# Kernel optimization log

Measured on AMD Instinct MI355X. Metric: run time of the kernel, lower is better.

The kernel has to match this reference:

```python
import math
import jax, jax.numpy as jnp
import numpy as np

DIM = 1024
QK_DIM = 200
HIDDEN = 2 * DIM  # expansion_factor = 2
N = 8192


def setup_inputs() -> dict:
    key = jax.random.key(0)
    ks = jax.random.split(key, 8)
    s = 0.02
    return {
        "x": jax.random.normal(ks[0], (N, DIM), dtype=jnp.float32),
        "W_hidden": jax.random.normal(ks[1], (DIM, 2 * HIDDEN), dtype=jnp.float32) * s,
        "b_hidden": jnp.zeros((2 * HIDDEN,), dtype=jnp.float32),
        "W_qk": jax.random.normal(ks[2], (DIM, QK_DIM), dtype=jnp.float32) * s,
        "b_qk": jnp.zeros((QK_DIM,), dtype=jnp.float32),
        "gamma": 1.0 + jax.random.normal(ks[3], (2, QK_DIM), dtype=jnp.float32) * s,
        "beta": jnp.zeros((2, QK_DIM), dtype=jnp.float32),
        "W_out": jax.random.normal(ks[4], (HIDDEN, DIM), dtype=jnp.float32) * s,
        "b_out": jnp.zeros((DIM,), dtype=jnp.float32),
    }


def reference(x, W_hidden, b_hidden, W_qk, b_qk, gamma, beta, W_out, b_out):
    # to_hidden: Linear(dim -> 2*hidden) + SiLU, then chunk into v, gate
    hid = jax.nn.silu(x @ W_hidden + b_hidden)        # [N, 2H]
    v, gate = jnp.split(hid, 2, axis=-1)              # [N, H] each
    # to_qk: Linear(dim -> qk_dim) + SiLU
    qk = jax.nn.silu(x @ W_qk + b_qk)                 # [N, qk]
    # OffsetScale (heads=2): per-head affine on the shared qk
    q = qk * gamma[0] + beta[0]                       # [N, qk]
    k = qk * gamma[1] + beta[1]                       # [N, qk]
    # scores scaled by sqrt(dim) (module uses self.dim, not qk_dim)
    sim = (q @ k.T) * (1.0 / math.sqrt(x.shape[-1]))  # [N, N]
    # ReLU-squared attention (no softmax); dropout=0.0 -> identity
    attn = jnp.square(jax.nn.relu(sim))
    out = attn @ v                                    # [N, H]
    out = out * gate
    out = out @ W_out + b_out                         # [N, dim]
    # add_residual=True in this module multiplies by x
    return out * x
```

## Files before the change

### kernel.cpp

```cpp
#include <hip/hip_runtime.h>
#include <stdint.h>


typedef __bf16 bf16x8 __attribute__((ext_vector_type(8)));
typedef float f32x4 __attribute__((ext_vector_type(4)));

__device__ __forceinline__ uint16_t f2bf(float f) {
  uint32_t u = __builtin_bit_cast(uint32_t, f);
  u += 0x7fffu + ((u >> 16) & 1u);
  return (uint16_t)(u >> 16);
}
__device__ __forceinline__ float silu_f(float s) {
  return s / (1.f + __expf(-s));
}

__device__ __forceinline__ void gload16(const void* g, void* l) {
  __builtin_amdgcn_global_load_lds(
      (__attribute__((address_space(1))) void*)const_cast<void*>(g),
      (__attribute__((address_space(3))) void*)l, 16, 0, 0);
}


__global__ void cast_to_bf16(const float* __restrict__ in, uint16_t* __restrict__ out, int n4) {
  int i = blockIdx.x * blockDim.x + threadIdx.x;
  if (i < n4) {
    float4 f = ((const float4*)in)[i];
    ushort4 o;
    o.x = f2bf(f.x); o.y = f2bf(f.y); o.z = f2bf(f.z); o.w = f2bf(f.w);
    ((ushort4*)out)[i] = o;
  }
}

__global__ void transpose_cast_pad(const float* __restrict__ in, uint16_t* __restrict__ out,
                                   int R, int C, int Cp) {
  __shared__ float tile[32][33];
  int cb = blockIdx.x * 32;
  int rb = blockIdx.y * 32;
  int tx = threadIdx.x;
  int ty = threadIdx.y;
#pragma unroll
  for (int i = 0; i < 4; ++i) {
    int r = rb + ty + i * 8;
    int c = cb + tx;
    tile[ty + i * 8][tx] = (c < C) ? in[(size_t)r * C + c] : 0.f;
  }
  __syncthreads();
#pragma unroll
  for (int i = 0; i < 4; ++i) {
    int c = cb + ty + i * 8;
    if (c < Cp) out[(size_t)c * R + rb + tx] = f2bf(tile[tx][ty + i * 8]);
  }
}


struct EpiParams {
  const float* bias;
  const float* bias2;
  const float* g0;
  const float* b0;
  const float* g1;
  const float* b1;
  const uint16_t* gate;
  const float* x;
  uint16_t* o16a;
  uint16_t* o16b;
  uint16_t* oq;
  uint16_t* ok;
  float* o32;
};

__global__ __launch_bounds__(256) void k_hidqk(
    const uint16_t* __restrict__ A, const uint16_t* __restrict__ Bt, EpiParams p) {
  __shared__ __align__(16) uint16_t SH[128 * 64];
  uint16_t* As = SH;
  uint16_t* Bs = SH + 4096;

  const int tid = threadIdx.x;
  const int lane = tid & 63;
  const int wave = tid >> 6;
  const int wr = (wave >> 1) * 64;
  const int wc = (wave & 1) * 64;
  const int m0 = blockIdx.y * 128;
  const int n0 = blockIdx.x * 128;
  const int lda = 1024, ldb = 1024, K = 1024;

  f32x4 acc[4][4] = {};

  const int r0 = tid >> 2;
  const int q8 = (tid & 3) * 8;
  const uint16_t* gA0 = A + (size_t)(m0 + r0) * lda + q8;
  const uint16_t* gA1 = A + (size_t)(m0 + 64 + r0) * lda + q8;
  const uint16_t* gB0 = Bt + (size_t)(n0 + r0) * ldb + q8;
  const uint16_t* gB1 = Bt + (size_t)(n0 + 64 + r0) * ldb + q8;
  uint16_t* lA0 = As + wave * 512;
  uint16_t* lA1 = As + 2048 + wave * 512;
  uint16_t* lB0 = Bs + wave * 512;
  uint16_t* lB1 = Bs + 2048 + wave * 512;

  const int fr = lane & 15;
  const int rg = lane >> 4;
  const int kq = rg * 8;

  for (int k0 = 0; k0 < K; k0 += 32) {
    __syncthreads();
    gload16(gA0 + k0, lA0);
    gload16(gA1 + k0, lA1);
    gload16(gB0 + k0, lB0);
    gload16(gB1 + k0, lB1);
    __syncthreads();

    bf16x8 a[4], b[4];
#pragma unroll
    for (int i = 0; i < 4; ++i)
      a[i] = *(const bf16x8*)(As + (wr + i * 16 + fr) * 32 + kq);
#pragma unroll
    for (int j = 0; j < 4; ++j)
      b[j] = *(const bf16x8*)(Bs + (wc + j * 16 + fr) * 32 + kq);
#pragma unroll
    for (int i = 0; i < 4; ++i)
#pragma unroll
      for (int j = 0; j < 4; ++j)
        acc[i][j] = __builtin_amdgcn_mfma_f32_16x16x32_bf16(a[i], b[j], acc[i][j], 0, 0, 0);
  }

  if (n0 < 2048) {
    __syncthreads();
    uint16_t* ar = SH + wave * 2048;
    const int lrow = lane >> 3;
    const int mc = (lane & 7) * 8;
#pragma unroll
    for (int j = 0; j < 4; ++j) {
      const float bc = p.bias[n0 + wc + j * 16 + fr];
#pragma unroll
      for (int i = 0; i < 4; ++i)
#pragma unroll
        for (int r = 0; r < 4; ++r)
          ar[fr * 72 + i * 16 + rg * 4 + r] = f2bf(silu_f(acc[i][j][r] + bc));
#pragma unroll
      for (int rr = 0; rr < 2; ++rr) {
        bf16x8 v = *(const bf16x8*)(ar + (rr * 8 + lrow) * 72 + mc);
        *(bf16x8*)(p.o16a + (size_t)(n0 + wc + j * 16 + rr * 8 + lrow) * 8192 + m0 + wr + mc) = v;
      }
    }
  } else if (n0 < 4096) {
    __syncthreads();
    uint16_t* ar = SH + wave * 2048;
    const int lrow = lane >> 3;
    const int nc = (lane & 7) * 8;
    float bc[4];
#pragma unroll
    for (int j = 0; j < 4; ++j) bc[j] = p.bias[n0 + wc + j * 16 + fr];
#pragma unroll
    for (int i = 0; i < 4; ++i) {
#pragma unroll
      for (int j = 0; j < 4; ++j)
#pragma unroll
        for (int r = 0; r < 4; ++r)
          ar[(rg * 4 + r) * 72 + j * 16 + fr] = f2bf(silu_f(acc[i][j][r] + bc[j]));
#pragma unroll
      for (int rr = 0; rr < 2; ++rr) {
        bf16x8 v = *(const bf16x8*)(ar + (rr * 8 + lrow) * 72 + nc);
        *(bf16x8*)(p.o16b + (size_t)(m0 + wr + i * 16 + rr * 8 + lrow) * 2048 + (n0 - 2048) + wc + nc) = v;
      }
    }
  } else {
#pragma unroll
    for (int i = 0; i < 4; ++i) {
#pragma unroll
      for (int j = 0; j < 4; ++j) {
        const int row = m0 + wr + i * 16 + rg * 4;
        const int qc = n0 + wc + j * 16 + fr - 4096;
        if (qc < 224) {
#pragma unroll
          for (int r = 0; r < 4; ++r) {
            float qv = 0.f, kv = 0.f;
            if (qc < 200) {
              float s = silu_f(acc[i][j][r] + p.bias2[qc]);
              qv = s * p.g0[qc] + p.b0[qc];
              kv = s * p.g1[qc] + p.b1[qc];
            }
            p.oq[(size_t)(row + r) * 224 + qc] = f2bf(qv);
            p.ok[(size_t)(row + r) * 224 + qc] = f2bf(kv);
          }
        }
      }
    }
  }
}

__global__ __launch_bounds__(256) void k_attn(
    const uint16_t* __restrict__ Q,
    const uint16_t* __restrict__ Kt,
    uint16_t* __restrict__ attn) {
  __shared__ __align__(16) uint16_t As[128 * 32];
  __shared__ __align__(16) uint16_t Bs[128 * 32];
  __shared__ __align__(16) uint16_t Ep[4][2][16 * 72];

  const int tid = threadIdx.x;
  const int lane = tid & 63;
  const int wave = tid >> 6;
  const int wr = (wave >> 1) * 64;
  const int wc = (wave & 1) * 64;
  const int m0 = blockIdx.y * 128;
  const int n0 = blockIdx.x * 128;
  const int lda = 224, ldb = 224, K = 224;

  f32x4 acc[4][4] = {};

  const int r0 = tid >> 2;
  const int q8 = (tid & 3) * 8;
  const uint16_t* gA0 = Q + (size_t)(m0 + r0) * lda + q8;
  const uint16_t* gA1 = Q + (size_t)(m0 + 64 + r0) * lda + q8;
  const uint16_t* gB0 = Kt + (size_t)(n0 + r0) * ldb + q8;
  const uint16_t* gB1 = Kt + (size_t)(n0 + 64 + r0) * ldb + q8;
  uint16_t* lA0 = As + wave * 512;
  uint16_t* lA1 = As + 2048 + wave * 512;
  uint16_t* lB0 = Bs + wave * 512;
  uint16_t* lB1 = Bs + 2048 + wave * 512;

  const int fr = lane & 15;
  const int rg = lane >> 4;
  const int kq = rg * 8;

  for (int k0 = 0; k0 < K; k0 += 32) {
    __syncthreads();
    gload16(gA0 + k0, lA0);
    gload16(gA1 + k0, lA1);
    gload16(gB0 + k0, lB0);
    gload16(gB1 + k0, lB1);
    __syncthreads();

    bf16x8 a[4], b[4];
#pragma unroll
    for (int i = 0; i < 4; ++i)
      a[i] = *(const bf16x8*)(As + (wr + i * 16 + fr) * 32 + kq);
#pragma unroll
    for (int j = 0; j < 4; ++j)
      b[j] = *(const bf16x8*)(Bs + (wc + j * 16 + fr) * 32 + kq);
#pragma unroll
    for (int i = 0; i < 4; ++i)
#pragma unroll
      for (int j = 0; j < 4; ++j)
        acc[i][j] = __builtin_amdgcn_mfma_f32_16x16x32_bf16(a[i], b[j], acc[i][j], 0, 0, 0);
  }

#pragma unroll
  for (int i = 0; i < 4; ++i) {
    uint16_t* sl = Ep[wave][i & 1];
#pragma unroll
    for (int j = 0; j < 4; ++j)
#pragma unroll
      for (int r = 0; r < 4; ++r) {
        float s = fmaxf(acc[i][j][r] * 0.03125f, 0.f);
        sl[(rg * 4 + r) * 72 + j * 16 + fr] = f2bf(s * s);
      }
    const int row = lane >> 2;
    const int c0 = (lane & 3) * 16;
    bf16x8 v0 = *(const bf16x8*)(sl + row * 72 + c0);
    bf16x8 v1 = *(const bf16x8*)(sl + row * 72 + c0 + 8);
    uint16_t* dst = attn + (size_t)(m0 + wr + i * 16 + row) * 8192 + (n0 + wc + c0);
    *(bf16x8*)(dst) = v0;
    *(bf16x8*)(dst + 8) = v1;
  }
}

__global__ __launch_bounds__(512, 2) void k_pv(
    const uint16_t* __restrict__ A, int lda,
    const uint16_t* __restrict__ Bt, int ldb,
    int K, int nx, EpiParams p) {
  __shared__ __align__(16) uint16_t SH[65536];

  const int id = blockIdx.x;
  const int bx = (id >> 3) % nx;
  const int by = (id & 7) + 8 * (id / (8 * nx));
  const int m0 = by * 256;
  const int n0 = bx * 256;

  const int tid = threadIdx.x;
  const int lane = tid & 63;
  const int wave = tid >> 6;
  const int wrM = (wave >> 2) * 128;
  const int wcN = (wave & 3) * 64;

  const int fr = lane & 15;
  const int rg = lane >> 4;
  const int swz = (rg ^ ((fr >> 1) & 3)) * 8;

  const int rdA = (wrM + fr) * 32 + swz;
  const int rdB = 8192 + (wcN + fr) * 32 + swz;

  const int srow = lane >> 2;
  const int sk = ((lane & 3) ^ ((lane >> 3) & 3)) * 8;
  const uint16_t* gA0 = A + (size_t)(m0 + wave * 16 + srow) * lda + sk;
  const uint16_t* gA1 = gA0 + (size_t)128 * lda;
  const uint16_t* gB0 = Bt + (size_t)(n0 + wave * 16 + srow) * ldb + sk;
  const uint16_t* gB1 = gB0 + (size_t)128 * ldb;

  f32x4 acc[8][4] = {};
  const int NT = K >> 5;

  for (int s = 0; s < 3; ++s) {
    const int ko = s * 32;
    uint16_t* d = SH + s * 16384 + wave * 512;
    gload16(gA0 + ko, d);
    gload16(gA1 + ko, d + 4096);
    gload16(gB0 + ko, d + 8192);
    gload16(gB1 + ko, d + 12288);
  }
  asm volatile("s_waitcnt vmcnt(8)" ::: "memory");
  __builtin_amdgcn_sched_barrier(0);
  __builtin_amdgcn_s_barrier();
  __builtin_amdgcn_sched_barrier(0);

#define PV_TILE(T_, B_, BS_)                                                   \
  do {                                                                         \
    const uint16_t* bA_ = SH + (B_) * 16384;                                   \
    const int kp_ = (((T_) + 3) & (NT - 1)) * 32;                              \
    uint16_t* sd_ = SH + (BS_) * 16384 + wave * 512;                           \
    bf16x8 aq[4], bq[4];                                                       \
    _Pragma("unroll") for (int j = 0; j < 4; ++j)                              \
        bq[j] = *(const bf16x8*)(bA_ + rdB + j * 512);                         \
    _Pragma("unroll") for (int i = 0; i < 4; ++i)                              \
        aq[i] = *(const bf16x8*)(bA_ + rdA + i * 512);                         \
    gload16(gA0 + kp_, sd_);                                                   \
    gload16(gA1 + kp_, sd_ + 4096);                                            \
    __builtin_amdgcn_s_setprio(1);                                             \
    _Pragma("unroll") for (int i = 0; i < 4; ++i)                              \
      _Pragma("unroll") for (int j = 0; j < 4; ++j)                            \
          acc[i][j] = __builtin_amdgcn_mfma_f32_16x16x32_bf16(                 \
              aq[i], bq[j], acc[i][j], 0, 0, 0);                               \
    __builtin_amdgcn_s_setprio(0);                                             \
    __builtin_amdgcn_sched_barrier(0);                                         \
    __builtin_amdgcn_s_barrier();                                              \
    __builtin_amdgcn_sched_barrier(0);                                         \
    _Pragma("unroll") for (int i = 0; i < 4; ++i)                              \
        aq[i] = *(const bf16x8*)(bA_ + rdA + (4 + i) * 512);                   \
    gload16(gB0 + kp_, sd_ + 8192);                                            \
    gload16(gB1 + kp_, sd_ + 12288);                                           \
    __builtin_amdgcn_s_setprio(1);                                             \
    _Pragma("unroll") for (int i = 0; i < 4; ++i)                              \
      _Pragma("unroll") for (int j = 0; j < 4; ++j)                            \
          acc[4 + i][j] = __builtin_amdgcn_mfma_f32_16x16x32_bf16(             \
              aq[i], bq[j], acc[4 + i][j], 0, 0, 0);                           \
    __builtin_amdgcn_s_setprio(0);                                             \
    asm volatile("s_waitcnt vmcnt(8)" ::: "memory");                           \
    __builtin_amdgcn_sched_barrier(0);                                         \
    __builtin_amdgcn_s_barrier();                                              \
    __builtin_amdgcn_sched_barrier(0);                                         \
  } while (0)

  for (int t0 = 0; t0 < NT; t0 += 4) {
    PV_TILE(t0 + 0, 0, 3);
    PV_TILE(t0 + 1, 1, 0);
    PV_TILE(t0 + 2, 2, 1);
    PV_TILE(t0 + 3, 3, 2);
  }
#undef PV_TILE

  asm volatile("s_waitcnt vmcnt(0)" ::: "memory");
  __builtin_amdgcn_sched_barrier(0);
  __builtin_amdgcn_s_barrier();
  __builtin_amdgcn_sched_barrier(0);

  uint16_t* ar = SH + wave * 2048;
  const int lrow = lane >> 3;
  const int nc = (lane & 7) * 8;
#pragma unroll
  for (int i = 0; i < 8; ++i) {
#pragma unroll
    for (int j = 0; j < 4; ++j)
#pragma unroll
      for (int r = 0; r < 4; ++r)
        ar[(rg * 4 + r) * 72 + j * 16 + fr] = f2bf(acc[i][j][r]);
#pragma unroll
    for (int rr = 0; rr < 2; ++rr) {
      const size_t base = (size_t)(m0 + wrM + i * 16 + rr * 8 + lrow) * 2048 + n0 + wcN + nc;
      bf16x8 v = *(const bf16x8*)(ar + (rr * 8 + lrow) * 72 + nc);
      bf16x8 g = *(const bf16x8*)(p.gate + base);
      bf16x8 o;
#pragma unroll
      for (int e = 0; e < 8; ++e) o[e] = (__bf16)((float)v[e] * (float)g[e]);
      *(bf16x8*)(p.o16a + base) = o;
    }
  }
}

__global__ __launch_bounds__(256) void k_final(
    const uint16_t* __restrict__ A,
    const uint16_t* __restrict__ Bt, EpiParams p) {
  __shared__ __align__(16) uint16_t As[128 * 32];
  __shared__ __align__(16) uint16_t Bs[128 * 32];

  const int tid = threadIdx.x;
  const int lane = tid & 63;
  const int wave = tid >> 6;
  const int wr = (wave >> 1) * 64;
  const int wc = (wave & 1) * 64;
  const int m0 = blockIdx.y * 128;
  const int n0 = blockIdx.x * 128;
  const int lda = 2048, ldb = 2048, K = 2048;

  f32x4 acc[4][4] = {};

  const int r0 = tid >> 2;
  const int q8 = (tid & 3) * 8;
  const uint16_t* gA0 = A + (size_t)(m0 + r0) * lda + q8;
  const uint16_t* gA1 = A + (size_t)(m0 + 64 + r0) * lda + q8;
  const uint16_t* gB0 = Bt + (size_t)(n0 + r0) * ldb + q8;
  const uint16_t* gB1 = Bt + (size_t)(n0 + 64 + r0) * ldb + q8;
  uint16_t* lA0 = As + wave * 512;
  uint16_t* lA1 = As + 2048 + wave * 512;
  uint16_t* lB0 = Bs + wave * 512;
  uint16_t* lB1 = Bs + 2048 + wave * 512;

  const int fr = lane & 15;
  const int kq = (lane >> 4) * 8;

  for (int k0 = 0; k0 < K; k0 += 32) {
    __syncthreads();
    gload16(gA0 + k0, lA0);
    gload16(gA1 + k0, lA1);
    gload16(gB0 + k0, lB0);
    gload16(gB1 + k0, lB1);
    __syncthreads();

    bf16x8 a[4], b[4];
#pragma unroll
    for (int i = 0; i < 4; ++i)
      a[i] = *(const bf16x8*)(As + (wr + i * 16 + fr) * 32 + kq);
#pragma unroll
    for (int j = 0; j < 4; ++j)
      b[j] = *(const bf16x8*)(Bs + (wc + j * 16 + fr) * 32 + kq);
#pragma unroll
    for (int i = 0; i < 4; ++i)
#pragma unroll
      for (int j = 0; j < 4; ++j)
        acc[i][j] = __builtin_amdgcn_mfma_f32_16x16x32_bf16(a[i], b[j], acc[i][j], 0, 0, 0);
  }

#pragma unroll
  for (int i = 0; i < 4; ++i) {
#pragma unroll
    for (int j = 0; j < 4; ++j) {
      const int row = m0 + wr + i * 16 + (lane >> 4) * 4;
      const int col = n0 + wc + j * 16 + fr;
      const float bc = p.bias[col];
#pragma unroll
      for (int r = 0; r < 4; ++r) {
        size_t idx = (size_t)(row + r) * 1024 + col;
        p.o32[idx] = (acc[i][j][r] + bc) * p.x[idx];
      }
    }
  }
}


extern "C" void kernel_launch(void* const* d_in, const int* in_sizes, int n_in,
                              void* d_out, int out_size, void* d_ws, size_t ws_size,
                              hipStream_t stream) {
  const float* x        = (const float*)d_in[0];
  const float* W_hidden = (const float*)d_in[1];
  const float* b_hidden = (const float*)d_in[2];
  const float* W_qk     = (const float*)d_in[3];
  const float* b_qk     = (const float*)d_in[4];
  const float* gamma    = (const float*)d_in[5];
  const float* beta     = (const float*)d_in[6];
  const float* W_out    = (const float*)d_in[7];
  const float* b_out    = (const float*)d_in[8];
  float* out = (float*)d_out;

  const bool fullM = ws_size >= (236ull << 20);
  const size_t region0 = fullM ? (128ull << 20) : (64ull << 20);

  char* base = (char*)d_ws;
  uint16_t* xb    = (uint16_t*)(base);
  uint16_t* WhT   = (uint16_t*)(base + (16ull << 20));
  uint16_t* WqkT  = (uint16_t*)(base + (24ull << 20));
  uint16_t* attnB = (uint16_t*)(base);
  char* tail = base + region0;
  uint16_t* WoT   = (uint16_t*)(tail);
  uint16_t* q     = (uint16_t*)(tail + (4ull << 20));
  uint16_t* kk    = (uint16_t*)(tail + (8ull << 20));
  uint16_t* vT    = (uint16_t*)(tail + (12ull << 20));
  uint16_t* gate  = (uint16_t*)(tail + (44ull << 20));
  uint16_t* out2g = (uint16_t*)(tail + (76ull << 20));
  (void)in_sizes; (void)n_in; (void)out_size;

  cast_to_bf16<<<(8192 * 1024 / 4) / 256, 256, 0, stream>>>(x, xb, 8192 * 1024 / 4);
  transpose_cast_pad<<<dim3(4096 / 32, 1024 / 32), dim3(32, 8), 0, stream>>>(W_hidden, WhT, 1024, 4096, 4096);
  transpose_cast_pad<<<dim3(256 / 32, 1024 / 32), dim3(32, 8), 0, stream>>>(W_qk, WqkT, 1024, 200, 256);
  transpose_cast_pad<<<dim3(1024 / 32, 2048 / 32), dim3(32, 8), 0, stream>>>(W_out, WoT, 2048, 1024, 1024);

  {
    EpiParams p{};
    p.bias = b_hidden; p.bias2 = b_qk;
    p.g0 = gamma; p.b0 = beta; p.g1 = gamma + 200; p.b1 = beta + 200;
    p.o16a = vT; p.o16b = gate; p.oq = q; p.ok = kk;
    k_hidqk<<<dim3(34, 64), 256, 0, stream>>>(xb, WhT, p);
  }

  if (fullM) {
    k_attn<<<dim3(64, 64), 256, 0, stream>>>(q, kk, attnB);
    {
      EpiParams p{};
      p.gate = gate; p.o16a = out2g;
      k_pv<<<dim3(8 * 32), 512, 0, stream>>>(attnB, 8192, vT, 8192, 8192, 8, p);
    }
  } else {
    for (int s = 0; s < 2; ++s) {
      k_attn<<<dim3(64, 32), 256, 0, stream>>>(q + (size_t)s * 4096 * 224, kk, attnB);
      {
        EpiParams p{};
        p.gate = gate + (size_t)s * 4096 * 2048;
        p.o16a = out2g + (size_t)s * 4096 * 2048;
        k_pv<<<dim3(8 * 16), 512, 0, stream>>>(attnB, 8192, vT, 8192, 8192, 8, p);
      }
    }
  }

  {
    EpiParams p{};
    p.bias = b_out; p.x = x; p.o32 = out;
    k_final<<<dim3(8, 64), 256, 0, stream>>>(out2g, WoT, p);
  }
}
```

Measured before the change: 598.7 us.

## Add 4-stage LDS ring pipeline with swizzle to hidqk, attn and final GEMMs

Replaces the simple two-barrier load/compute loop in k_hidqk, k_attn and k_final with a 4-buffer LDS ring. Global-to-LDS loads run three tiles ahead, reads use an XOR-swizzled layout, and MFMA runs under raised priority. The Q/K row stride is padded from 224 to 256 so the ring's power-of-two tile count works, and the k_pv macro is simplified to issue all loads up front with 8 A fragments. This aims to hide global load latency and cut LDS bank conflicts, at the cost of more LDS per block and extra zero-padding traffic for Q/K.

```diff
diff --git a/kernel.cpp b/kernel.cpp
--- a/kernel.cpp
+++ b/kernel.cpp
@@ -69,11 +69,59 @@
   float* o32;
 };
 
-__global__ __launch_bounds__(256) void k_hidqk(
+#define TILE128(T_, B_, BS_)                                                   \
+  do {                                                                         \
+    const uint16_t* base_ = SH + (B_) * 8192;                                  \
+    const int kp_ = (((T_) + 3) & (NT - 1)) * 32;                              \
+    uint16_t* sd_ = SH + (BS_) * 8192 + wave * 512;                            \
+    gload16(gA0 + kp_, sd_);                                                   \
+    gload16(gA1 + kp_, sd_ + 2048);                                            \
+    gload16(gB0 + kp_, sd_ + 4096);                                            \
+    gload16(gB1 + kp_, sd_ + 6144);                                            \
+    bf16x8 a_[4], b_[4];                                                       \
+    _Pragma("unroll") for (int j = 0; j < 4; ++j)                              \
+        b_[j] = *(const bf16x8*)(base_ + rdB + j * 512);                       \
+    _Pragma("unroll") for (int i = 0; i < 4; ++i)                              \
+        a_[i] = *(const bf16x8*)(base_ + rdA + i * 512);                       \
+    __builtin_amdgcn_s_setprio(1);                                             \
+    _Pragma("unroll") for (int i = 0; i < 4; ++i)                              \
+      _Pragma("unroll") for (int j = 0; j < 4; ++j)                            \
+          acc[i][j] = __builtin_amdgcn_mfma_f32_16x16x32_bf16(                 \
+              a_[i], b_[j], acc[i][j], 0, 0, 0);                               \
+    __builtin_amdgcn_s_setprio(0);                                             \
+    asm volatile("s_waitcnt vmcnt(8)" ::: "memory");                           \
+    __builtin_amdgcn_sched_barrier(0);                                         \
+    __builtin_amdgcn_s_barrier();                                              \
+    __builtin_amdgcn_sched_barrier(0);                                         \
+  } while (0)
+
+#define RING_LOOP128()                                                         \
+  do {                                                                         \
+    _Pragma("unroll") for (int s_ = 0; s_ < 3; ++s_) {                         \
+      uint16_t* d_ = SH + s_ * 8192 + wave * 512;                              \
+      gload16(gA0 + s_ * 32, d_);                                              \
+      gload16(gA1 + s_ * 32, d_ + 2048);                                       \
+      gload16(gB0 + s_ * 32, d_ + 4096);                                       \
+      gload16(gB1 + s_ * 32, d_ + 6144);                                       \
+    }                                                                          \
+    asm volatile("s_waitcnt vmcnt(8)" ::: "memory");                           \
+    __builtin_amdgcn_sched_barrier(0);                                         \
+    __builtin_amdgcn_s_barrier();                                              \
+    __builtin_amdgcn_sched_barrier(0);                                         \
+    for (int t0_ = 0; t0_ < NT; t0_ += 4) {                                    \
+      TILE128(t0_ + 0, 0, 3);                                                  \
+      TILE128(t0_ + 1, 1, 0);                                                  \
+      TILE128(t0_ + 2, 2, 1);                                                  \
+      TILE128(t0_ + 3, 3, 2);                                                  \
+    }                                                                          \
+    asm volatile("s_waitcnt vmcnt(0)" ::: "memory");                           \
+    __builtin_amdgcn_sched_barrier(0);                                         \
+    __syncthreads();                                                           \
+  } while (0)
+
+__global__ __launch_bounds__(256, 2) void k_hidqk(
     const uint16_t* __restrict__ A, const uint16_t* __restrict__ Bt, EpiParams p) {
-  __shared__ __align__(16) uint16_t SH[128 * 64];
-  uint16_t* As = SH;
-  uint16_t* Bs = SH + 4096;
+  __shared__ __align__(16) uint16_t SH[32768];
 
   const int tid = threadIdx.x;
   const int lane = tid & 63;
@@ -82,49 +130,27 @@
   const int wc = (wave & 1) * 64;
   const int m0 = blockIdx.y * 128;
   const int n0 = blockIdx.x * 128;
-  const int lda = 1024, ldb = 1024, K = 1024;
+  const int lda = 1024, ldb = 1024;
+  const int NT = 32;
 
   f32x4 acc[4][4] = {};
-
-  const int r0 = tid >> 2;
-  const int q8 = (tid & 3) * 8;
-  const uint16_t* gA0 = A + (size_t)(m0 + r0) * lda + q8;
-  const uint16_t* gA1 = A + (size_t)(m0 + 64 + r0) * lda + q8;
-  const uint16_t* gB0 = Bt + (size_t)(n0 + r0) * ldb + q8;
-  const uint16_t* gB1 = Bt + (size_t)(n0 + 64 + r0) * ldb + q8;
-  uint16_t* lA0 = As + wave * 512;
-  uint16_t* lA1 = As + 2048 + wave * 512;
-  uint16_t* lB0 = Bs + wave * 512;
-  uint16_t* lB1 = Bs + 2048 + wave * 512;
 
   const int fr = lane & 15;
   const int rg = lane >> 4;
-  const int kq = rg * 8;
-
-  for (int k0 = 0; k0 < K; k0 += 32) {
-    __syncthreads();
-    gload16(gA0 + k0, lA0);
-    gload16(gA1 + k0, lA1);
-    gload16(gB0 + k0, lB0);
-    gload16(gB1 + k0, lB1);
-    __syncthreads();
-
-    bf16x8 a[4], b[4];
-#pragma unroll
-    for (int i = 0; i < 4; ++i)
-      a[i] = *(const bf16x8*)(As + (wr + i * 16 + fr) * 32 + kq);
-#pragma unroll
-    for (int j = 0; j < 4; ++j)
-      b[j] = *(const bf16x8*)(Bs + (wc + j * 16 + fr) * 32 + kq);
-#pragma unroll
-    for (int i = 0; i < 4; ++i)
-#pragma unroll
-      for (int j = 0; j < 4; ++j)
-        acc[i][j] = __builtin_amdgcn_mfma_f32_16x16x32_bf16(a[i], b[j], acc[i][j], 0, 0, 0);
-  }
+  const int swz = (rg ^ ((fr >> 1) & 3)) * 8;
+  const int rdA = (wr + fr) * 32 + swz;
+  const int rdB = 4096 + (wc + fr) * 32 + swz;
+
+  const int srow = lane >> 2;
+  const int sk = ((lane & 3) ^ ((lane >> 3) & 3)) * 8;
+  const uint16_t* gA0 = A + (size_t)(m0 + wave * 16 + srow) * lda + sk;
+  const uint16_t* gA1 = gA0 + (size_t)64 * lda;
+  const uint16_t* gB0 = Bt + (size_t)(n0 + wave * 16 + srow) * ldb + sk;
+  const uint16_t* gB1 = gB0 + (size_t)64 * ldb;
+
+  RING_LOOP128();
 
   if (n0 < 2048) {
-    __syncthreads();
     uint16_t* ar = SH + wave * 2048;
     const int lrow = lane >> 3;
     const int mc = (lane & 7) * 8;
@@ -143,7 +169,6 @@
       }
     }
   } else if (n0 < 4096) {
-    __syncthreads();
     uint16_t* ar = SH + wave * 2048;
     const int lrow = lane >> 3;
     const int nc = (lane & 7) * 8;
@@ -170,31 +195,27 @@
       for (int j = 0; j < 4; ++j) {
         const int row = m0 + wr + i * 16 + rg * 4;
         const int qc = n0 + wc + j * 16 + fr - 4096;
-        if (qc < 224) {
-#pragma unroll
-          for (int r = 0; r < 4; ++r) {
-            float qv = 0.f, kv = 0.f;
-            if (qc < 200) {
-              float s = silu_f(acc[i][j][r] + p.bias2[qc]);
-              qv = s * p.g0[qc] + p.b0[qc];
-              kv = s * p.g1[qc] + p.b1[qc];
-            }
-            p.oq[(size_t)(row + r) * 224 + qc] = f2bf(qv);
-            p.ok[(size_t)(row + r) * 224 + qc] = f2bf(kv);
+#pragma unroll
+        for (int r = 0; r < 4; ++r) {
+          float qv = 0.f, kv = 0.f;
+          if (qc < 200) {
+            float s = silu_f(acc[i][j][r] + p.bias2[qc]);
+            qv = s * p.g0[qc] + p.b0[qc];
+            kv = s * p.g1[qc] + p.b1[qc];
           }
+          p.oq[(size_t)(row + r) * 256 + qc] = f2bf(qv);
+          p.ok[(size_t)(row + r) * 256 + qc] = f2bf(kv);
         }
       }
     }
   }
 }
 
-__global__ __launch_bounds__(256) void k_attn(
+__global__ __launch_bounds__(256, 2) void k_attn(
     const uint16_t* __restrict__ Q,
     const uint16_t* __restrict__ Kt,
     uint16_t* __restrict__ attn) {
-  __shared__ __align__(16) uint16_t As[128 * 32];
-  __shared__ __align__(16) uint16_t Bs[128 * 32];
-  __shared__ __align__(16) uint16_t Ep[4][2][16 * 72];
+  __shared__ __align__(16) uint16_t SH[32768];
 
   const int tid = threadIdx.x;
   const int lane = tid & 63;
@@ -203,50 +224,29 @@
   const int wc = (wave & 1) * 64;
   const int m0 = blockIdx.y * 128;
   const int n0 = blockIdx.x * 128;
-  const int lda = 224, ldb = 224, K = 224;
+  const int lda = 256, ldb = 256;
+  const int NT = 8;
 
   f32x4 acc[4][4] = {};
-
-  const int r0 = tid >> 2;
-  const int q8 = (tid & 3) * 8;
-  const uint16_t* gA0 = Q + (size_t)(m0 + r0) * lda + q8;
-  const uint16_t* gA1 = Q + (size_t)(m0 + 64 + r0) * lda + q8;
-  const uint16_t* gB0 = Kt + (size_t)(n0 + r0) * ldb + q8;
-  const uint16_t* gB1 = Kt + (size_t)(n0 + 64 + r0) * ldb + q8;
-  uint16_t* lA0 = As + wave * 512;
-  uint16_t* lA1 = As + 2048 + wave * 512;
-  uint16_t* lB0 = Bs + wave * 512;
-  uint16_t* lB1 = Bs + 2048 + wave * 512;
 
   const int fr = lane & 15;
   const int rg = lane >> 4;
-  const int kq = rg * 8;
-
-  for (int k0 = 0; k0 < K; k0 += 32) {
-    __syncthreads();
-    gload16(gA0 + k0, lA0);
-    gload16(gA1 + k0, lA1);
-    gload16(gB0 + k0, lB0);
-    gload16(gB1 + k0, lB1);
-    __syncthreads();
-
-    bf16x8 a[4], b[4];
-#pragma unroll
-    for (int i = 0; i < 4; ++i)
-      a[i] = *(const bf16x8*)(As + (wr + i * 16 + fr) * 32 + kq);
-#pragma unroll
-    for (int j = 0; j < 4; ++j)
-      b[j] = *(const bf16x8*)(Bs + (wc + j * 16 + fr) * 32 + kq);
-#pragma unroll
-    for (int i = 0; i < 4; ++i)
-#pragma unroll
-      for (int j = 0; j < 4; ++j)
-        acc[i][j] = __builtin_amdgcn_mfma_f32_16x16x32_bf16(a[i], b[j], acc[i][j], 0, 0, 0);
-  }
+  const int swz = (rg ^ ((fr >> 1) & 3)) * 8;
+  const int rdA = (wr + fr) * 32 + swz;
+  const int rdB = 4096 + (wc + fr) * 32 + swz;
+
+  const int srow = lane >> 2;
+  const int sk = ((lane & 3) ^ ((lane >> 3) & 3)) * 8;
+  const uint16_t* gA0 = Q + (size_t)(m0 + wave * 16 + srow) * lda + sk;
+  const uint16_t* gA1 = gA0 + (size_t)64 * lda;
+  const uint16_t* gB0 = Kt + (size_t)(n0 + wave * 16 + srow) * ldb + sk;
+  const uint16_t* gB1 = gB0 + (size_t)64 * ldb;
+
+  RING_LOOP128();
 
 #pragma unroll
   for (int i = 0; i < 4; ++i) {
-    uint16_t* sl = Ep[wave][i & 1];
+    uint16_t* sl = SH + wave * 4096 + (i & 1) * 2048;
 #pragma unroll
     for (int j = 0; j < 4; ++j)
 #pragma unroll
@@ -317,31 +317,20 @@
     const uint16_t* bA_ = SH + (B_) * 16384;                                   \
     const int kp_ = (((T_) + 3) & (NT - 1)) * 32;                              \
     uint16_t* sd_ = SH + (BS_) * 16384 + wave * 512;                           \
-    bf16x8 aq[4], bq[4];                                                       \
+    gload16(gA0 + kp_, sd_);                                                   \
+    gload16(gA1 + kp_, sd_ + 4096);                                            \
+    gload16(gB0 + kp_, sd_ + 8192);                                            \
+    gload16(gB1 + kp_, sd_ + 12288);                                           \
+    bf16x8 aq[8], bq[4];                                                       \
     _Pragma("unroll") for (int j = 0; j < 4; ++j)                              \
         bq[j] = *(const bf16x8*)(bA_ + rdB + j * 512);                         \
-    _Pragma("unroll") for (int i = 0; i < 4; ++i)                              \
+    _Pragma("unroll") for (int i = 0; i < 8; ++i)                              \
         aq[i] = *(const bf16x8*)(bA_ + rdA + i * 512);                         \
-    gload16(gA0 + kp_, sd_);                                                   \
-    gload16(gA1 + kp_, sd_ + 4096);                                            \
     __builtin_amdgcn_s_setprio(1);                                             \
-    _Pragma("unroll") for (int i = 0; i < 4; ++i)                              \
+    _Pragma("unroll") for (int i = 0; i < 8; ++i)                              \
       _Pragma("unroll") for (int j = 0; j < 4; ++j)                            \
           acc[i][j] = __builtin_amdgcn_mfma_f32_16x16x32_bf16(                 \
               aq[i], bq[j], acc[i][j], 0, 0, 0);                               \
-    __builtin_amdgcn_s_setprio(0);                                             \
-    __builtin_amdgcn_sched_barrier(0);                                         \
-    __builtin_amdgcn_s_barrier();                                              \
-    __builtin_amdgcn_sched_barrier(0);                                         \
-    _Pragma("unroll") for (int i = 0; i < 4; ++i)                              \
-        aq[i] = *(const bf16x8*)(bA_ + rdA + (4 + i) * 512);                   \
-    gload16(gB0 + kp_, sd_ + 8192);                                            \
-    gload16(gB1 + kp_, sd_ + 12288);                                           \
-    __builtin_amdgcn_s_setprio(1);                                             \
-    _Pragma("unroll") for (int i = 0; i < 4; ++i)                              \
-      _Pragma("unroll") for (int j = 0; j < 4; ++j)                            \
-          acc[4 + i][j] = __builtin_amdgcn_mfma_f32_16x16x32_bf16(             \
-              aq[i], bq[j], acc[4 + i][j], 0, 0, 0);                           \
     __builtin_amdgcn_s_setprio(0);                                             \
     asm volatile("s_waitcnt vmcnt(8)" ::: "memory");                           \
     __builtin_amdgcn_sched_barrier(0);                                         \
@@ -385,11 +374,10 @@
   }
 }
 
-__global__ __launch_bounds__(256) void k_final(
+__global__ __launch_bounds__(256, 2) void k_final(
     const uint16_t* __restrict__ A,
     const uint16_t* __restrict__ Bt, EpiParams p) {
-  __shared__ __align__(16) uint16_t As[128 * 32];
-  __shared__ __align__(16) uint16_t Bs[128 * 32];
+  __shared__ __align__(16) uint16_t SH[32768];
 
   const int tid = threadIdx.x;
   const int lane = tid & 63;
@@ -398,51 +386,31 @@
   const int wc = (wave & 1) * 64;
   const int m0 = blockIdx.y * 128;
   const int n0 = blockIdx.x * 128;
-  const int lda = 2048, ldb = 2048, K = 2048;
+  const int lda = 2048, ldb = 2048;
+  const int NT = 64;
 
   f32x4 acc[4][4] = {};
 
-  const int r0 = tid >> 2;
-  const int q8 = (tid & 3) * 8;
-  const uint16_t* gA0 = A + (size_t)(m0 + r0) * lda + q8;
-  const uint16_t* gA1 = A + (size_t)(m0 + 64 + r0) * lda + q8;
-  const uint16_t* gB0 = Bt + (size_t)(n0 + r0) * ldb + q8;
-  const uint16_t* gB1 = Bt + (size_t)(n0 + 64 + r0) * ldb + q8;
-  uint16_t* lA0 = As + wave * 512;
-  uint16_t* lA1 = As + 2048 + wave * 512;
-  uint16_t* lB0 = Bs + wave * 512;
-  uint16_t* lB1 = Bs + 2048 + wave * 512;
-
   const int fr = lane & 15;
-  const int kq = (lane >> 4) * 8;
-
-  for (int k0 = 0; k0 < K; k0 += 32) {
-    __syncthreads();
-    gload16(gA0 + k0, lA0);
-    gload16(gA1 + k0, lA1);
-    gload16(gB0 + k0, lB0);
-    gload16(gB1 + k0, lB1);
-    __syncthreads();
-
-    bf16x8 a[4], b[4];
-#pragma unroll
-    for (int i = 0; i < 4; ++i)
-      a[i] = *(const bf16x8*)(As + (wr + i * 16 + fr) * 32 + kq);
-#pragma unroll
-    for (int j = 0; j < 4; ++j)
-      b[j] = *(const bf16x8*)(Bs + (wc + j * 16 + fr) * 32 + kq);
-#pragma unroll
-    for (int i = 0; i < 4; ++i)
-#pragma unroll
-      for (int j = 0; j < 4; ++j)
-        acc[i][j] = __builtin_amdgcn_mfma_f32_16x16x32_bf16(a[i], b[j], acc[i][j], 0, 0, 0);
-  }
+  const int rg = lane >> 4;
+  const int swz = (rg ^ ((fr >> 1) & 3)) * 8;
+  const int rdA = (wr + fr) * 32 + swz;
+  const int rdB = 4096 + (wc + fr) * 32 + swz;
+
+  const int srow = lane >> 2;
+  const int sk = ((lane & 3) ^ ((lane >> 3) & 3)) * 8;
+  const uint16_t* gA0 = A + (size_t)(m0 + wave * 16 + srow) * lda + sk;
+  const uint16_t* gA1 = gA0 + (size_t)64 * lda;
+  const uint16_t* gB0 = Bt + (size_t)(n0 + wave * 16 + srow) * ldb + sk;
+  const uint16_t* gB1 = gB0 + (size_t)64 * ldb;
+
+  RING_LOOP128();
 
 #pragma unroll
   for (int i = 0; i < 4; ++i) {
 #pragma unroll
     for (int j = 0; j < 4; ++j) {
-      const int row = m0 + wr + i * 16 + (lane >> 4) * 4;
+      const int row = m0 + wr + i * 16 + rg * 4;
       const int col = n0 + wc + j * 16 + fr;
       const float bc = p.bias[col];
 #pragma unroll
@@ -508,7 +476,7 @@
     }
   } else {
     for (int s = 0; s < 2; ++s) {
-      k_attn<<<dim3(64, 32), 256, 0, stream>>>(q + (size_t)s * 4096 * 224, kk, attnB);
+      k_attn<<<dim3(64, 32), 256, 0, stream>>>(q + (size_t)s * 4096 * 256, kk, attnB);
       {
         EpiParams p{};
         p.gate = gate + (size_t)s * 4096 * 2048;
```

Result: faster. 570.5 us (-4.7%).
